# Optimization experiments

Hardware: AMD Instinct MI355X
Metric: run time of the kernel (lower is better)

Reference implementation:

```python
import jax, jax.numpy as jnp
import numpy as np

HEAD_DIM = 128
NUM_HEADS = 16
NUM_KV_HEADS = 8
HIDDEN = 2048
SEQ = 4096
BATCH = 1
ROPE_THETA = 1e6
RMS_EPS = 1e-6


def rms_norm(x, w, eps=RMS_EPS):
    # normalize over the last (head_dim) axis
    var = jnp.mean(jnp.square(x), axis=-1, keepdims=True)
    return x * jax.lax.rsqrt(var + eps) * w


def apply_rope(x, positions):
    # x: [B, S, H, D], positions: [B, S]; rotate-half (GPT-NeoX style)
    d = x.shape[-1]
    inv_freq = 1.0 / (ROPE_THETA ** (jnp.arange(0, d, 2, dtype=jnp.float32) / d))  # [D/2]
    ang = positions.astype(jnp.float32)[..., None] * inv_freq  # [B, S, D/2]
    cos = jnp.cos(ang)[:, :, None, :]  # [B, S, 1, D/2]
    sin = jnp.sin(ang)[:, :, None, :]
    x1, x2 = x[..., : d // 2], x[..., d // 2 :]
    return jnp.concatenate([x1 * cos - x2 * sin, x2 * cos + x1 * sin], axis=-1)


def setup_inputs() -> dict:
    key = jax.random.key(0)
    ks = jax.random.split(key, 8)
    s = 0.02
    return {
        "positions": jnp.broadcast_to(jnp.arange(SEQ, dtype=jnp.int64 if jax.config.jax_enable_x64 else jnp.int32)[None, :], (BATCH, SEQ)),
        "hidden_states": jax.random.normal(ks[0], (BATCH, SEQ, HIDDEN), jnp.float32),
        "wq": jax.random.normal(ks[1], (NUM_HEADS * HEAD_DIM, HIDDEN), jnp.float32) * s,
        "bq": jnp.zeros((NUM_HEADS * HEAD_DIM,), jnp.float32),
        "wk": jax.random.normal(ks[2], (NUM_KV_HEADS * HEAD_DIM, HIDDEN), jnp.float32) * s,
        "bk": jnp.zeros((NUM_KV_HEADS * HEAD_DIM,), jnp.float32),
        "wv": jax.random.normal(ks[3], (NUM_KV_HEADS * HEAD_DIM, HIDDEN), jnp.float32) * s,
        "bv": jnp.zeros((NUM_KV_HEADS * HEAD_DIM,), jnp.float32),
        "wo": jax.random.normal(ks[4], (HIDDEN, NUM_HEADS * HEAD_DIM), jnp.float32) * s,
        "bo": jnp.zeros((HIDDEN,), jnp.float32),
        "q_norm_w": jnp.ones((HEAD_DIM,), jnp.float32),
        "k_norm_w": jnp.ones((HEAD_DIM,), jnp.float32),
    }


def reference(positions, hidden_states, wq, bq, wk, bk, wv, bv, wo, bo, q_norm_w, k_norm_w):
    B, S, _ = hidden_states.shape
    H, Hkv, D = NUM_HEADS, NUM_KV_HEADS, HEAD_DIM
    scaling = D ** -0.5

    q = (hidden_states @ wq.T + bq).reshape(B, S, H, D)
    k = (hidden_states @ wk.T + bk).reshape(B, S, Hkv, D)
    v = (hidden_states @ wv.T + bv).reshape(B, S, Hkv, D)

    q = apply_rope(rms_norm(q, q_norm_w), positions)
    k = apply_rope(rms_norm(k, k_norm_w), positions)

    # GQA: repeat_interleave kv heads to match query heads
    rep = H // Hkv
    k = jnp.repeat(k, rep, axis=2)  # [B, S, H, D]
    v = jnp.repeat(v, rep, axis=2)

    # scores: [B, H, S, S]
    scores = jnp.einsum("bqhd,bkhd->bhqk", q, k) * scaling
    causal = jnp.tril(jnp.ones((S, S), dtype=bool))
    scores = jnp.where(causal[None, None], scores, -jnp.inf)
    attn = jax.nn.softmax(scores, axis=-1)

    out = jnp.einsum("bhqk,bkhd->bqhd", attn, v).reshape(B, S, H * D)
    return out @ wo.T + bo
```

## Files before the change

### kernel.cpp

```cpp
#include <hip/hip_runtime.h>
#include <hip/hip_bf16.h>

#define SQ   4096
#define HIDN 2048
#define NH   16
#define NKV  8
#define HD   128
#define QD   2048
#define KD   1024
#define KVB  64

typedef __bf16 bf16x8 __attribute__((ext_vector_type(8)));
typedef float  f32x4  __attribute__((ext_vector_type(4)));

__device__ __forceinline__ float b2f(unsigned short u) {
    union { float f; unsigned int i; } v; v.i = ((unsigned int)u) << 16; return v.f;
}
__device__ __forceinline__ unsigned short f2b(float f) {
    union { float f; unsigned int i; } v; v.f = f;
    unsigned int i = v.i;
    return (unsigned short)((i + 0x7FFFu + ((i >> 16) & 1u)) >> 16);
}

__device__ __forceinline__ void gload_lds16(const void* g, void* l) {
    __builtin_amdgcn_global_load_lds(
        (const __attribute__((address_space(1))) unsigned int*)g,
        (__attribute__((address_space(3))) unsigned int*)l, 16, 0, 0);
}

#define MFMA16(a, b, c) __builtin_amdgcn_mfma_f32_16x16x32_bf16(a, b, c, 0, 0, 0)

#define DPP_ROR(x, n) __int_as_float(__builtin_amdgcn_update_dpp(            \
    __float_as_int(x), __float_as_int(x), 0x120 + (n), 0xF, 0xF, false))

__device__ __forceinline__ float rowmax16(float x) {
    x = fmaxf(x, DPP_ROR(x, 1));
    x = fmaxf(x, DPP_ROR(x, 2));
    x = fmaxf(x, DPP_ROR(x, 4));
    x = fmaxf(x, DPP_ROR(x, 8));
    return x;
}
__device__ __forceinline__ float rowsum16(float x) {
    x += DPP_ROR(x, 1);
    x += DPP_ROR(x, 2);
    x += DPP_ROR(x, 4);
    x += DPP_ROR(x, 8);
    return x;
}

__global__ __launch_bounds__(256) void cvt_all(const float* __restrict__ h,
                                               const float* __restrict__ wq,
                                               const float* __restrict__ wk,
                                               const float* __restrict__ wv,
                                               const float* __restrict__ wo,
                                               unsigned short* __restrict__ oh,
                                               unsigned short* __restrict__ owq,
                                               unsigned short* __restrict__ owk,
                                               unsigned short* __restrict__ owv,
                                               unsigned short* __restrict__ owo) {
    int i = blockIdx.x * 256 + threadIdx.x;
    const float* src; unsigned short* dst; int off;
    if (i < 2097152)      { src = h;  dst = oh;  off = i; }
    else if (i < 3145728) { src = wq; dst = owq; off = i - 2097152; }
    else if (i < 3670016) { src = wk; dst = owk; off = i - 3145728; }
    else if (i < 4194304) { src = wv; dst = owv; off = i - 3670016; }
    else                  { src = wo; dst = owo; off = i - 4194304; }
    float4 v = ((const float4*)src)[off];
    ushort4 u;
    u.x = f2b(v.x); u.y = f2b(v.y); u.z = f2b(v.z); u.w = f2b(v.w);
    ((ushort4*)dst)[off] = u;
}

__global__ __launch_bounds__(256) void rope_table(const int* __restrict__ pos,
                                                  float* __restrict__ cosT,
                                                  float* __restrict__ sinT) {
    int i = blockIdx.x * 256 + threadIdx.x;
    int s = i >> 6, j = i & 63;
    double invf = exp(-(double)j * (log(1.0e6) / 64.0));
    float a = (float)((double)pos[s] * invf);
    cosT[i] = cosf(a);
    sinT[i] = sinf(a);
}

template <int EPI>
__global__ __launch_bounds__(256) void gemm128(const unsigned short* __restrict__ A,
                                               const unsigned short* __restrict__ B,
                                               const float* __restrict__ bias,
                                               void* __restrict__ Cout,
                                               int M, int N, int K) {
    __shared__ unsigned short As[128 * 32];
    __shared__ unsigned short Bs[128 * 32];
    const int tid = threadIdx.x, wid = tid >> 6, lane = tid & 63;
    const int g = lane >> 4, c = lane & 15;
    const int wr = wid >> 1, wc = wid & 1;
    const int orig = blockIdx.y * gridDim.x + blockIdx.x;
    const int cpx = (gridDim.x * gridDim.y) >> 3;
    const int wg = (orig & 7) * cpx + (orig >> 3);
    const int bx = wg % gridDim.x, by = wg / gridDim.x;
    const long rowbase = (long)by * 128;
    const long colbase = (long)bx * 128;

    f32x4 acc[4][4];
#pragma unroll
    for (int m = 0; m < 4; ++m)
#pragma unroll
        for (int n = 0; n < 4; ++n) acc[m][n] = (f32x4){0.f, 0.f, 0.f, 0.f};

    const int ch0 = (wid * 2) * 64 + lane;
    const int ch1 = (wid * 2 + 1) * 64 + lane;

    for (int kt = 0; kt < K; kt += 32) {
        gload_lds16(A + ((rowbase + (ch0 >> 2)) * K + kt + (ch0 & 3) * 8),
                    As + (wid * 2) * 64 * 8);
        gload_lds16(B + ((colbase + (ch0 >> 2)) * K + kt + (ch0 & 3) * 8),
                    Bs + (wid * 2) * 64 * 8);
        gload_lds16(A + ((rowbase + (ch1 >> 2)) * K + kt + (ch1 & 3) * 8),
                    As + (wid * 2 + 1) * 64 * 8);
        gload_lds16(B + ((colbase + (ch1 >> 2)) * K + kt + (ch1 & 3) * 8),
                    Bs + (wid * 2 + 1) * 64 * 8);
        __syncthreads();
        bf16x8 a[4], b[4];
#pragma unroll
        for (int m = 0; m < 4; ++m)
            a[m] = *(const bf16x8*)(As + (wr * 64 + m * 16 + c) * 32 + g * 8);
#pragma unroll
        for (int n = 0; n < 4; ++n)
            b[n] = *(const bf16x8*)(Bs + (wc * 64 + n * 16 + c) * 32 + g * 8);
#pragma unroll
        for (int m = 0; m < 4; ++m)
#pragma unroll
            for (int n = 0; n < 4; ++n) acc[m][n] = MFMA16(a[m], b[n], acc[m][n]);
        __syncthreads();
    }

#pragma unroll
    for (int m = 0; m < 4; ++m) {
        const long grow0 = rowbase + wr * 64 + m * 16 + g * 4;
#pragma unroll
        for (int n = 0; n < 4; ++n) {
            const long gcol = colbase + wc * 64 + n * 16 + c;
            const float bs = bias[gcol];
            if (EPI == 0) {
                unsigned short* C = (unsigned short*)Cout;
#pragma unroll
                for (int r = 0; r < 4; ++r)
                    C[(grow0 + r) * N + gcol] = f2b(acc[m][n][r] + bs);
            } else if (EPI == 1) {
                float* C = (float*)Cout;
#pragma unroll
                for (int r = 0; r < 4; ++r)
                    C[(grow0 + r) * N + gcol] = acc[m][n][r] + bs;
            } else {
                unsigned short* C = (unsigned short*)Cout;
                ushort4 pk;
                pk.x = f2b(acc[m][n][0] + bs);
                pk.y = f2b(acc[m][n][1] + bs);
                pk.z = f2b(acc[m][n][2] + bs);
                pk.w = f2b(acc[m][n][3] + bs);
                *(ushort4*)(C + gcol * (long)M + grow0) = pk;
            }
        }
    }
}

__global__ __launch_bounds__(256) void norm_rope(const unsigned short* __restrict__ proj,
                                                 int nh,
                                                 const float* __restrict__ w,
                                                 const float* __restrict__ cosT,
                                                 const float* __restrict__ sinT,
                                                 unsigned short* __restrict__ outt,
                                                 float oscale) {
    int wv = (blockIdx.x * 256 + threadIdx.x) >> 6;
    int lane = threadIdx.x & 63;
    int s = wv / nh, h = wv - s * nh;
    const unsigned short* p = proj + (size_t)s * (nh * HD) + h * HD;
    float x1 = b2f(p[lane]);
    float x2 = b2f(p[lane + 64]);
    float ss = x1 * x1 + x2 * x2;
#pragma unroll
    for (int d = 1; d < 64; d <<= 1) ss += __shfl_xor(ss, d);
    float r = rsqrtf(ss * (1.f / 128.f) + 1e-6f);
    x1 *= r * w[lane];
    x2 *= r * w[lane + 64];
    float cs = cosT[s * 64 + lane], sn = sinT[s * 64 + lane];
    unsigned short o1 = f2b((x1 * cs - x2 * sn) * oscale);
    unsigned short o2 = f2b((x2 * cs + x1 * sn) * oscale);
    unsigned short* q = outt + ((size_t)h * SQ + s) * HD;
    q[lane] = o1;
    q[lane + 64] = o2;
}

__global__ __launch_bounds__(256, 2) void fattn(const unsigned short* __restrict__ qt,
                                                const unsigned short* __restrict__ kt,
                                                const unsigned short* __restrict__ vt,
                                                unsigned short* __restrict__ aout) {
    __shared__ unsigned short Ks[2][KVB * HD];
    __shared__ unsigned short Vs[2][HD * KVB];
    __shared__ unsigned short Pl[4][32][64];
    const int tid = threadIdx.x, wid = tid >> 6, lane = tid & 63;
    const int g = lane >> 4, c = lane & 15;
    const int id = blockIdx.x;
    const int qb = (id < 256) ? (id >> 4) : (31 - ((id - 256) >> 4));
    const int h = id & 15, hk = h >> 1;
    const int qrow0 = qb * 128 + wid * 32;
    const unsigned short* qh = qt + (size_t)h * SQ * HD;
    const unsigned short* kh = kt + (size_t)hk * SQ * HD;
    const unsigned short* vh = vt + (size_t)hk * HD * SQ;
    const int ntile = 2 * qb + 2;
    char* plw = (char*)&Pl[wid][0][0];

    bf16x8 qa[2][4];
#pragma unroll
    for (int m = 0; m < 2; ++m)
#pragma unroll
        for (int ks = 0; ks < 4; ++ks)
            qa[m][ks] = *(const bf16x8*)(qh + (size_t)(qrow0 + m * 16 + c) * HD + ks * 32 + g * 8);

    f32x4 o[2][8];
#pragma unroll
    for (int m = 0; m < 2; ++m)
#pragma unroll
        for (int df = 0; df < 8; ++df) o[m][df] = (f32x4){0.f, 0.f, 0.f, 0.f};
    float mrow[2][4], lrow[2][4];
#pragma unroll
    for (int m = 0; m < 2; ++m)
#pragma unroll
        for (int r = 0; r < 4; ++r) { mrow[m][r] = -1e30f; lrow[m][r] = 0.f; }

    auto stage = [&](int b, int t) {
        const int kv0 = t * KVB;
#pragma unroll
        for (int i = 0; i < 4; ++i) {
            const int gi = wid * 4 + i;
            const int P = gi * 1024 + lane * 16;
            const int rk = P >> 8;
            const int Uk = (P & 255) ^ (((rk >> 2) & 7) << 4);
            gload_lds16(kh + (size_t)(kv0 + rk) * HD + (Uk >> 1),
                        (char*)Ks[b] + gi * 1024);
            const int rv = P >> 7;
            const int Uv = (P & 127) ^ ((rv & 7) << 4);
            gload_lds16(vh + (size_t)rv * SQ + kv0 + (Uv >> 1),
                        (char*)Vs[b] + gi * 1024);
        }
    };

    stage(0, 0);
    asm volatile("s_waitcnt vmcnt(0)" ::: "memory");
    __syncthreads();

    int bcur = 0;
    for (int j = 0; j < ntile; ++j) {
        const int kv0 = j * KVB;
        if (j + 1 < ntile) stage(bcur ^ 1, j + 1);

        if (kv0 <= qrow0 + 31) {
            f32x4 sa[2][4];
#pragma unroll
            for (int m = 0; m < 2; ++m)
#pragma unroll
                for (int nf = 0; nf < 4; ++nf) sa[m][nf] = (f32x4){0.f, 0.f, 0.f, 0.f};
            __builtin_amdgcn_s_setprio(1);
#pragma unroll
            for (int nf = 0; nf < 4; ++nf) {
                const int row = (c << 2) + nf;
                const int key = (c & 7) << 4;
#pragma unroll
                for (int ks = 0; ks < 4; ++ks) {
                    bf16x8 kf = *(const bf16x8*)((const char*)Ks[bcur] + row * 256 +
                                                 ((ks * 64 + g * 16) ^ key));
                    sa[0][nf] = MFMA16(qa[0][ks], kf, sa[0][nf]);
                    sa[1][nf] = MFMA16(qa[1][ks], kf, sa[1][nf]);
                }
            }
            __builtin_amdgcn_s_setprio(0);
            if (kv0 + 63 > qrow0) {
#pragma unroll
                for (int m = 0; m < 2; ++m)
#pragma unroll
                    for (int nf = 0; nf < 4; ++nf) {
                        const int col = kv0 + (c << 2) + nf;
#pragma unroll
                        for (int r = 0; r < 4; ++r) {
                            int row = qrow0 + m * 16 + g * 4 + r;
                            if (col > row) sa[m][nf][r] = -1e30f;
                        }
                    }
            }
            float nmax[2][4];
            int small = 1;
#pragma unroll
            for (int m = 0; m < 2; ++m)
#pragma unroll
                for (int r = 0; r < 4; ++r) {
                    float mx = fmaxf(fmaxf(sa[m][0][r], sa[m][1][r]),
                                     fmaxf(sa[m][2][r], sa[m][3][r]));
                    mx = rowmax16(mx);
                    nmax[m][r] = mx;
                    small &= (mx <= mrow[m][r] + 8.0f);
                }
            if (!__all(small)) {
                float psc[2][4];
#pragma unroll
                for (int m = 0; m < 2; ++m)
#pragma unroll
                    for (int r = 0; r < 4; ++r) {
                        float mn = fmaxf(mrow[m][r], nmax[m][r]);
                        psc[m][r] = __builtin_amdgcn_exp2f(mrow[m][r] - mn);
                        mrow[m][r] = mn;
                        lrow[m][r] *= psc[m][r];
                    }
#pragma unroll
                for (int m = 0; m < 2; ++m)
#pragma unroll
                    for (int df = 0; df < 8; ++df)
#pragma unroll
                        for (int r = 0; r < 4; ++r) o[m][df][r] *= psc[m][r];
            }
#pragma unroll
            for (int m = 0; m < 2; ++m)
#pragma unroll
                for (int r = 0; r < 4; ++r) {
                    float rs = 0.f;
#pragma unroll
                    for (int nf = 0; nf < 4; ++nf) {
                        float p = __builtin_amdgcn_exp2f(sa[m][nf][r] - mrow[m][r]);
                        sa[m][nf][r] = p;
                        rs += p;
                    }
                    lrow[m][r] += rowsum16(rs);
                }
#pragma unroll
            for (int m = 0; m < 2; ++m)
#pragma unroll
                for (int r = 0; r < 4; ++r) {
                    unsigned int lo, hi;
                    asm("v_cvt_pk_bf16_f32 %0, %1, %2"
                        : "=v"(lo) : "v"(sa[m][0][r]), "v"(sa[m][1][r]));
                    asm("v_cvt_pk_bf16_f32 %0, %1, %2"
                        : "=v"(hi) : "v"(sa[m][2][r]), "v"(sa[m][3][r]));
                    const int row = m * 16 + g * 4 + r;
                    const int pcol = (c * 8) ^ ((row & 7) << 4);
                    *(uint2*)(plw + row * 128 + pcol) = make_uint2(lo, hi);
                }
            __builtin_amdgcn_s_setprio(1);
#pragma unroll
            for (int ks = 0; ks < 2; ++ks) {
                bf16x8 pa0 = *(const bf16x8*)(plw + (0 * 16 + c) * 128 +
                                              ((ks * 64 + g * 16) ^ ((c & 7) << 4)));
                bf16x8 pa1 = *(const bf16x8*)(plw + (1 * 16 + c) * 128 +
                                              ((ks * 64 + g * 16) ^ ((c & 7) << 4)));
#pragma unroll
                for (int df = 0; df < 8; ++df) {
                    const int rd = df * 16 + c;
                    bf16x8 vb = *(const bf16x8*)((const char*)Vs[bcur] + rd * 128 +
                                                 ((ks * 64 + g * 16) ^ ((rd & 7) << 4)));
                    o[0][df] = MFMA16(pa0, vb, o[0][df]);
                    o[1][df] = MFMA16(pa1, vb, o[1][df]);
                }
            }
            __builtin_amdgcn_s_setprio(0);
        }
        asm volatile("s_waitcnt vmcnt(0)" ::: "memory");
        __syncthreads();
        bcur ^= 1;
    }

    float inv[2][4];
#pragma unroll
    for (int m = 0; m < 2; ++m)
#pragma unroll
        for (int r = 0; r < 4; ++r) inv[m][r] = 1.f / lrow[m][r];
#pragma unroll
    for (int m = 0; m < 2; ++m)
#pragma unroll
        for (int df = 0; df < 8; ++df)
#pragma unroll
            for (int r = 0; r < 4; ++r) {
                size_t row = qrow0 + m * 16 + g * 4 + r;
                aout[row * QD + h * HD + df * 16 + c] = f2b(o[m][df][r] * inv[m][r]);
            }
}

extern "C" void kernel_launch(void* const* d_in, const int* in_sizes, int n_in,
                              void* d_out, int out_size, void* d_ws, size_t ws_size,
                              hipStream_t stream) {
    const int*   positions = (const int*)d_in[0];
    const float* hidden    = (const float*)d_in[1];
    const float* wq        = (const float*)d_in[2];
    const float* bq        = (const float*)d_in[3];
    const float* wk        = (const float*)d_in[4];
    const float* bk        = (const float*)d_in[5];
    const float* wv        = (const float*)d_in[6];
    const float* bv        = (const float*)d_in[7];
    const float* wo        = (const float*)d_in[8];
    const float* bo        = (const float*)d_in[9];
    const float* qnw       = (const float*)d_in[10];
    const float* knw       = (const float*)d_in[11];
    float* out = (float*)d_out;

    char* w = (char*)d_ws;
    unsigned short* hidden_b = (unsigned short*)(w);
    unsigned short* wq_b     = (unsigned short*)(w + 16777216);
    unsigned short* wk_b     = (unsigned short*)(w + 25165824);
    unsigned short* wv_b     = (unsigned short*)(w + 29360128);
    unsigned short* wo_b     = (unsigned short*)(w + 33554432);
    unsigned short* qproj    = (unsigned short*)(w + 41943040);
    unsigned short* kproj    = (unsigned short*)(w + 58720256);
    unsigned short* q_t      = (unsigned short*)(w + 67108864);
    unsigned short* k_t      = (unsigned short*)(w + 83886080);
    unsigned short* v_t      = (unsigned short*)(w + 92274688);
    float*          cosT     = (float*)(w + 100663296);
    float*          sinT     = (float*)(w + 101711872);
    unsigned short* attn     = qproj;

    cvt_all<<<20480, 256, 0, stream>>>(hidden, wq, wk, wv, wo,
                                       hidden_b, wq_b, wk_b, wv_b, wo_b);
    rope_table<<<SQ * 64 / 256, 256, 0, stream>>>(positions, cosT, sinT);
    gemm128<0><<<dim3(QD / 128, SQ / 128), 256, 0, stream>>>(hidden_b, wq_b, bq, qproj, SQ, QD, HIDN);
    gemm128<0><<<dim3(KD / 128, SQ / 128), 256, 0, stream>>>(hidden_b, wk_b, bk, kproj, SQ, KD, HIDN);
    gemm128<2><<<dim3(KD / 128, SQ / 128), 256, 0, stream>>>(hidden_b, wv_b, bv, v_t, SQ, KD, HIDN);
    norm_rope<<<SQ * NH / 4, 256, 0, stream>>>(qproj, NH, qnw, cosT, sinT, q_t,
                                               (float)(0.08838834764831845 * 1.4426950408889634));
    norm_rope<<<SQ * NKV / 4, 256, 0, stream>>>(kproj, NKV, knw, cosT, sinT, k_t, 1.0f);
    fattn<<<512, 256, 0, stream>>>(q_t, k_t, v_t, attn);
    gemm128<1><<<dim3(QD / 128, SQ / 128), 256, 0, stream>>>(attn, wo_b, bo, out, SQ, QD, HIDN);
}
```

Before: 517.2 us.

## Pair causal query blocks per 512-thread attention workgroup and use float rope table

The flash-attention kernel now launches 256 workgroups of 8 waves. Each wave processes 16 rows from a low query block and 16 rows from the mirrored high block, so every workgroup does balanced causal work and shares each staged K/V tile across twice as many waves. Waves skip the low-block MFMAs once that block is past the diagonal. The rope table now computes inverse frequencies in float with __expf instead of double exp, which removes slow FP64 work but may shift the angles slightly at large positions.

Result: slower. 1.352 ms (+161.3%).

```diff
diff --git a/kernel.cpp b/kernel.cpp
--- a/kernel.cpp
+++ b/kernel.cpp
@@ -76,8 +76,8 @@
                                                   float* __restrict__ sinT) {
     int i = blockIdx.x * 256 + threadIdx.x;
     int s = i >> 6, j = i & 63;
-    double invf = exp(-(double)j * (log(1.0e6) / 64.0));
-    float a = (float)((double)pos[s] * invf);
+    float invf = __expf(-(float)j * (1.3815510557964274f / 6.4f));
+    float a = (float)pos[s] * invf;
     cosT[i] = cosf(a);
     sinT[i] = sinf(a);
 }
@@ -190,31 +190,31 @@
     q[lane + 64] = o2;
 }
 
-__global__ __launch_bounds__(256, 2) void fattn(const unsigned short* __restrict__ qt,
+__global__ __launch_bounds__(512, 2) void fattn(const unsigned short* __restrict__ qt,
                                                 const unsigned short* __restrict__ kt,
                                                 const unsigned short* __restrict__ vt,
                                                 unsigned short* __restrict__ aout) {
     __shared__ unsigned short Ks[2][KVB * HD];
     __shared__ unsigned short Vs[2][HD * KVB];
-    __shared__ unsigned short Pl[4][32][64];
+    __shared__ unsigned short Pl[8][32][64];
     const int tid = threadIdx.x, wid = tid >> 6, lane = tid & 63;
     const int g = lane >> 4, c = lane & 15;
     const int id = blockIdx.x;
-    const int qb = (id < 256) ? (id >> 4) : (31 - ((id - 256) >> 4));
-    const int h = id & 15, hk = h >> 1;
-    const int qrow0 = qb * 128 + wid * 32;
+    const int h = id & 15, qc = id >> 4, hk = h >> 1;
+    const int row0A = qc * 128 + wid * 16;
+    const int row0B = (31 - qc) * 128 + wid * 16;
     const unsigned short* qh = qt + (size_t)h * SQ * HD;
     const unsigned short* kh = kt + (size_t)hk * SQ * HD;
     const unsigned short* vh = vt + (size_t)hk * HD * SQ;
-    const int ntile = 2 * qb + 2;
+    const int ntile = 2 * (31 - qc) + 2;
     char* plw = (char*)&Pl[wid][0][0];
 
     bf16x8 qa[2][4];
 #pragma unroll
-    for (int m = 0; m < 2; ++m)
-#pragma unroll
-        for (int ks = 0; ks < 4; ++ks)
-            qa[m][ks] = *(const bf16x8*)(qh + (size_t)(qrow0 + m * 16 + c) * HD + ks * 32 + g * 8);
+    for (int ks = 0; ks < 4; ++ks) {
+        qa[0][ks] = *(const bf16x8*)(qh + (size_t)(row0A + c) * HD + ks * 32 + g * 8);
+        qa[1][ks] = *(const bf16x8*)(qh + (size_t)(row0B + c) * HD + ks * 32 + g * 8);
+    }
 
     f32x4 o[2][8];
 #pragma unroll
@@ -230,8 +230,8 @@
     auto stage = [&](int b, int t) {
         const int kv0 = t * KVB;
 #pragma unroll
-        for (int i = 0; i < 4; ++i) {
-            const int gi = wid * 4 + i;
+        for (int i = 0; i < 2; ++i) {
+            const int gi = wid * 2 + i;
             const int P = gi * 1024 + lane * 16;
             const int rk = P >> 8;
             const int Uk = (P & 255) ^ (((rk >> 2) & 7) << 4);
@@ -248,48 +248,67 @@
     asm volatile("s_waitcnt vmcnt(0)" ::: "memory");
     __syncthreads();
 
+#define QK_BODY(DO0)                                                          \
+    _Pragma("unroll") for (int nf = 0; nf < 4; ++nf) {                        \
+        const int krow = (c << 2) + nf;                                       \
+        const int key = (c & 7) << 4;                                         \
+        _Pragma("unroll") for (int ks = 0; ks < 4; ++ks) {                    \
+            bf16x8 kf = *(const bf16x8*)((const char*)Ks[bcur] + krow * 256 + \
+                                         ((ks * 64 + g * 16) ^ key));         \
+            if (DO0) sa[0][nf] = MFMA16(qa[0][ks], kf, sa[0][nf]);            \
+            sa[1][nf] = MFMA16(qa[1][ks], kf, sa[1][nf]);                     \
+        }                                                                     \
+    }
+
+#define PV_BODY(DO0)                                                          \
+    _Pragma("unroll") for (int ks = 0; ks < 2; ++ks) {                        \
+        const int pk_ = (ks * 64 + g * 16) ^ ((c & 7) << 4);                  \
+        bf16x8 pa1 = *(const bf16x8*)(plw + (16 + c) * 128 + pk_);            \
+        bf16x8 pa0{};                                                         \
+        if (DO0) pa0 = *(const bf16x8*)(plw + c * 128 + pk_);                 \
+        _Pragma("unroll") for (int df = 0; df < 8; ++df) {                    \
+            const int rd = df * 16 + c;                                       \
+            bf16x8 vb = *(const bf16x8*)((const char*)Vs[bcur] + rd * 128 +   \
+                                         ((ks * 64 + g * 16) ^ ((rd & 7) << 4))); \
+            if (DO0) o[0][df] = MFMA16(pa0, vb, o[0][df]);                    \
+            o[1][df] = MFMA16(pa1, vb, o[1][df]);                             \
+        }                                                                     \
+    }
+
     int bcur = 0;
     for (int j = 0; j < ntile; ++j) {
         const int kv0 = j * KVB;
         if (j + 1 < ntile) stage(bcur ^ 1, j + 1);
 
-        if (kv0 <= qrow0 + 31) {
+        const bool act0 = (kv0 <= row0A + 15);
+        const bool act1 = (kv0 <= row0B + 15);
+        if (act1) {
+            const int mlo = act0 ? 0 : 1;
             f32x4 sa[2][4];
 #pragma unroll
             for (int m = 0; m < 2; ++m)
 #pragma unroll
                 for (int nf = 0; nf < 4; ++nf) sa[m][nf] = (f32x4){0.f, 0.f, 0.f, 0.f};
             __builtin_amdgcn_s_setprio(1);
-#pragma unroll
-            for (int nf = 0; nf < 4; ++nf) {
-                const int row = (c << 2) + nf;
-                const int key = (c & 7) << 4;
-#pragma unroll
-                for (int ks = 0; ks < 4; ++ks) {
-                    bf16x8 kf = *(const bf16x8*)((const char*)Ks[bcur] + row * 256 +
-                                                 ((ks * 64 + g * 16) ^ key));
-                    sa[0][nf] = MFMA16(qa[0][ks], kf, sa[0][nf]);
-                    sa[1][nf] = MFMA16(qa[1][ks], kf, sa[1][nf]);
-                }
-            }
+            if (act0) { QK_BODY(1) } else { QK_BODY(0) }
             __builtin_amdgcn_s_setprio(0);
-            if (kv0 + 63 > qrow0) {
-#pragma unroll
-                for (int m = 0; m < 2; ++m)
+            const int rb[2] = {row0A, row0B};
+            for (int m = mlo; m < 2; ++m) {
+                if (kv0 + 63 > rb[m]) {
 #pragma unroll
                     for (int nf = 0; nf < 4; ++nf) {
                         const int col = kv0 + (c << 2) + nf;
 #pragma unroll
                         for (int r = 0; r < 4; ++r) {
-                            int row = qrow0 + m * 16 + g * 4 + r;
+                            int row = rb[m] + g * 4 + r;
                             if (col > row) sa[m][nf][r] = -1e30f;
                         }
                     }
+                }
             }
             float nmax[2][4];
             int small = 1;
-#pragma unroll
-            for (int m = 0; m < 2; ++m)
+            for (int m = mlo; m < 2; ++m)
 #pragma unroll
                 for (int r = 0; r < 4; ++r) {
                     float mx = fmaxf(fmaxf(sa[m][0][r], sa[m][1][r]),
@@ -299,25 +318,22 @@
                     small &= (mx <= mrow[m][r] + 8.0f);
                 }
             if (!__all(small)) {
-                float psc[2][4];
-#pragma unroll
-                for (int m = 0; m < 2; ++m)
+                for (int m = mlo; m < 2; ++m) {
+                    float psc[4];
 #pragma unroll
                     for (int r = 0; r < 4; ++r) {
                         float mn = fmaxf(mrow[m][r], nmax[m][r]);
-                        psc[m][r] = __builtin_amdgcn_exp2f(mrow[m][r] - mn);
+                        psc[r] = __builtin_amdgcn_exp2f(mrow[m][r] - mn);
                         mrow[m][r] = mn;
-                        lrow[m][r] *= psc[m][r];
+                        lrow[m][r] *= psc[r];
                     }
 #pragma unroll
-                for (int m = 0; m < 2; ++m)
-#pragma unroll
                     for (int df = 0; df < 8; ++df)
 #pragma unroll
-                        for (int r = 0; r < 4; ++r) o[m][df][r] *= psc[m][r];
+                        for (int r = 0; r < 4; ++r) o[m][df][r] *= psc[r];
+                }
             }
-#pragma unroll
-            for (int m = 0; m < 2; ++m)
+            for (int m = mlo; m < 2; ++m)
 #pragma unroll
                 for (int r = 0; r < 4; ++r) {
                     float rs = 0.f;
@@ -329,8 +345,7 @@
                     }
                     lrow[m][r] += rowsum16(rs);
                 }
-#pragma unroll
-            for (int m = 0; m < 2; ++m)
+            for (int m = mlo; m < 2; ++m)
 #pragma unroll
                 for (int r = 0; r < 4; ++r) {
                     unsigned int lo, hi;
@@ -343,21 +358,7 @@
                     *(uint2*)(plw + row * 128 + pcol) = make_uint2(lo, hi);
                 }
             __builtin_amdgcn_s_setprio(1);
-#pragma unroll
-            for (int ks = 0; ks < 2; ++ks) {
-                bf16x8 pa0 = *(const bf16x8*)(plw + (0 * 16 + c) * 128 +
-                                              ((ks * 64 + g * 16) ^ ((c & 7) << 4)));
-                bf16x8 pa1 = *(const bf16x8*)(plw + (1 * 16 + c) * 128 +
-                                              ((ks * 64 + g * 16) ^ ((c & 7) << 4)));
-#pragma unroll
-                for (int df = 0; df < 8; ++df) {
-                    const int rd = df * 16 + c;
-                    bf16x8 vb = *(const bf16x8*)((const char*)Vs[bcur] + rd * 128 +
-                                                 ((ks * 64 + g * 16) ^ ((rd & 7) << 4)));
-                    o[0][df] = MFMA16(pa0, vb, o[0][df]);
-                    o[1][df] = MFMA16(pa1, vb, o[1][df]);
-                }
-            }
+            if (act0) { PV_BODY(1) } else { PV_BODY(0) }
             __builtin_amdgcn_s_setprio(0);
         }
         asm volatile("s_waitcnt vmcnt(0)" ::: "memory");
@@ -365,20 +366,22 @@
         bcur ^= 1;
     }
 
-    float inv[2][4];
-#pragma unroll
-    for (int m = 0; m < 2; ++m)
-#pragma unroll
-        for (int r = 0; r < 4; ++r) inv[m][r] = 1.f / lrow[m][r];
-#pragma unroll
-    for (int m = 0; m < 2; ++m)
+    const int rb[2] = {row0A, row0B};
+#pragma unroll
+    for (int m = 0; m < 2; ++m) {
+        float inv[4];
+#pragma unroll
+        for (int r = 0; r < 4; ++r) inv[r] = 1.f / lrow[m][r];
 #pragma unroll
         for (int df = 0; df < 8; ++df)
 #pragma unroll
             for (int r = 0; r < 4; ++r) {
-                size_t row = qrow0 + m * 16 + g * 4 + r;
-                aout[row * QD + h * HD + df * 16 + c] = f2b(o[m][df][r] * inv[m][r]);
+                size_t row = rb[m] + g * 4 + r;
+                aout[row * QD + h * HD + df * 16 + c] = f2b(o[m][df][r] * inv[r]);
             }
+    }
+#undef QK_BODY
+#undef PV_BODY
 }
 
 extern "C" void kernel_launch(void* const* d_in, const int* in_sizes, int n_in,
@@ -422,6 +425,6 @@
     norm_rope<<<SQ * NH / 4, 256, 0, stream>>>(qproj, NH, qnw, cosT, sinT, q_t,
                                                (float)(0.08838834764831845 * 1.4426950408889634));
     norm_rope<<<SQ * NKV / 4, 256, 0, stream>>>(kproj, NKV, knw, cosT, sinT, k_t, 1.0f);
-    fattn<<<512, 256, 0, stream>>>(q_t, k_t, v_t, attn);
+    fattn<<<256, 512, 0, stream>>>(q_t, k_t, v_t, attn);
     gemm128<1><<<dim3(QD / 128, SQ / 128), 256, 0, stream>>>(attn, wo_b, bo, out, SQ, QD, HIDN);
 }
```
